# Kernel optimization log

Hardware: AMD Instinct MI355X
Metric: run time of the kernel (lower is better)

## Reference

```python
import jax, jax.numpy as jnp
import numpy as np

N_NODES = 100_000
N_EDGES = 800_000
D_IN = 64
HID = 32   # hidden_channels
OUT = 64   # out_channels
H1, H2, H3 = 7, 4, 1


def _lin(key, din, dout, scale=0.05):
    k1, k2 = jax.random.split(key)
    W = jax.random.normal(k1, (din, dout), jnp.float32) * scale
    b = jax.random.normal(k2, (dout,), jnp.float32) * scale
    return W, b


def setup_inputs() -> dict:
    key = jax.random.key(0)
    ks = jax.random.split(key, 16)
    x = jax.random.normal(ks[0], (N_NODES, D_IN), jnp.float32)
    edge_index = jax.random.randint(ks[1], (2, N_EDGES), 0, N_NODES, dtype=jnp.int32)
    inp = {"x": x, "edge_index": edge_index}
    # (in_dim, heads, per-head channels) for the 3 TransformerConv layers
    dims = [(D_IN, H1, HID), (H1 * HID, H2, HID), (H2 * HID, H3, OUT)]
    i = 2
    for l, (din, h, c) in enumerate(dims, start=1):
        for nm in ("q", "k", "v", "s"):  # query, key, value, skip linears
            W, b = _lin(ks[i], din, h * c)
            i += 1
            inp[f"W{nm}{l}"] = W
            inp[f"b{nm}{l}"] = b
    return inp


def _transformer_conv(x, src, dst, Wq, bq, Wk, bk, Wv, bv, Ws, bs, H, C):
    # PyG TransformerConv (concat=True, beta=False, root_weight=True, no edge feats)
    q = (x @ Wq + bq).reshape(-1, H, C)
    k = (x @ Wk + bk).reshape(-1, H, C)
    v = (x @ Wv + bv).reshape(-1, H, C)
    # per-edge attention logits [E, H]
    alpha = jnp.einsum('ehc,ehc->eh', q[dst], k[src]) / jnp.sqrt(jnp.asarray(C, q.dtype))
    # segment softmax over incoming edges of each dst node
    amax = jax.ops.segment_max(alpha, dst, num_segments=N_NODES)
    ex = jnp.exp(alpha - amax[dst])
    denom = jax.ops.segment_sum(ex, dst, num_segments=N_NODES)
    attn = ex / (denom[dst] + 1e-16)
    # weighted message aggregation [N, H, C] -> [N, H*C]
    msg = v[src] * attn[..., None]
    out = jax.ops.segment_sum(msg, dst, num_segments=N_NODES).reshape(N_NODES, H * C)
    # root/skip connection
    return out + x @ Ws + bs


def reference(x, edge_index,
              Wq1, bq1, Wk1, bk1, Wv1, bv1, Ws1, bs1,
              Wq2, bq2, Wk2, bk2, Wv2, bv2, Ws2, bs2,
              Wq3, bq3, Wk3, bk3, Wv3, bv3, Ws3, bs3):
    src, dst = edge_index[0], edge_index[1]
    h = jax.nn.relu(_transformer_conv(x, src, dst, Wq1, bq1, Wk1, bk1, Wv1, bv1, Ws1, bs1, H1, HID))
    h = jax.nn.relu(_transformer_conv(h, src, dst, Wq2, bq2, Wk2, bk2, Wv2, bv2, Ws2, bs2, H2, HID))
    return _transformer_conv(h, src, dst, Wq3, bq3, Wk3, bk3, Wv3, bv3, Ws3, bs3, H3, OUT)
```

## Files before the change

### kernel.cpp

```cpp
#include <hip/hip_runtime.h>
#include <hip/hip_bf16.h>
#include <math.h>

#define N_NODES 100000
#define N_EDGES 800000
#define SCAN_BLOCKS 98

typedef __attribute__((ext_vector_type(8))) short short8;
typedef __attribute__((ext_vector_type(4))) float f32x4;

__device__ __forceinline__ unsigned short f2b(float f) {
    __hip_bfloat16 h = __float2bfloat16(f);
    return *reinterpret_cast<unsigned short*>(&h);
}
__device__ __forceinline__ float b2f(unsigned short u) {
    unsigned int v = ((unsigned int)u) << 16;
    float f;
    __builtin_memcpy(&f, &v, 4);
    return f;
}
__device__ __forceinline__ float2 up2(unsigned u) {
    unsigned lo = u << 16;
    unsigned hi = u & 0xffff0000u;
    float2 r;
    __builtin_memcpy(&r.x, &lo, 4);
    __builtin_memcpy(&r.y, &hi, 4);
    return r;
}


__global__ void hist_kernel(const int* __restrict__ dst, int* __restrict__ deg) {
    int e = blockIdx.x * blockDim.x + threadIdx.x;
    if (e < N_EDGES) atomicAdd(&deg[dst[e]], 1);
}

__global__ __launch_bounds__(1024) void scan_part(const int* __restrict__ deg,
                                                  int* __restrict__ rowptr,
                                                  int* __restrict__ partials) {
    __shared__ int buf[1024];
    const int t = threadIdx.x;
    const int i = blockIdx.x * 1024 + t;
    int x = (i < N_NODES) ? deg[i] : 0;
    buf[t] = x;
    __syncthreads();
    for (int off = 1; off < 1024; off <<= 1) {
        int y = (t >= off) ? buf[t - off] : 0;
        __syncthreads();
        buf[t] += y;
        __syncthreads();
    }
    if (i < N_NODES) rowptr[i] = buf[t] - x;
    if (t == 1023) partials[blockIdx.x] = buf[t];
}

__global__ __launch_bounds__(128) void scan_tail(int* __restrict__ partials,
                                                 int* __restrict__ rowptr) {
    __shared__ int buf[128];
    const int t = threadIdx.x;
    int x = (t < SCAN_BLOCKS) ? partials[t] : 0;
    buf[t] = x;
    __syncthreads();
    for (int off = 1; off < 128; off <<= 1) {
        int y = (t >= off) ? buf[t - off] : 0;
        __syncthreads();
        buf[t] += y;
        __syncthreads();
    }
    if (t < SCAN_BLOCKS) partials[t] = buf[t] - x;
    if (t == 127) rowptr[N_NODES] = buf[127];
}

__global__ __launch_bounds__(1024) void scan_add(int* __restrict__ rowptr,
                                                 const int* __restrict__ partials) {
    const int i = blockIdx.x * 1024 + threadIdx.x;
    if (i < N_NODES) rowptr[i] += partials[blockIdx.x];
}

__global__ void scatter_kernel(const int* __restrict__ src, const int* __restrict__ dst,
                               const int* __restrict__ rowptr, int* __restrict__ cursor,
                               int* __restrict__ sorted_src) {
    int e = blockIdx.x * blockDim.x + threadIdx.x;
    if (e < N_EDGES) {
        int d = dst[e];
        int pos = atomicAdd(&cursor[d], 1);
        sorted_src[rowptr[d] + pos] = src[e];
    }
}

__global__ void fill_kernel(float* __restrict__ out, int n, float val) {
    int i = blockIdx.x * blockDim.x + threadIdx.x;
    if (i < n) out[i] = val;
}


__global__ void convert_kernel(const float* __restrict__ X, unsigned short* __restrict__ Y, int n4) {
    int i = blockIdx.x * blockDim.x + threadIdx.x;
    if (i < n4) {
        float4 f = ((const float4*)X)[i];
        ushort4 u;
        u.x = f2b(f.x); u.y = f2b(f.y); u.z = f2b(f.z); u.w = f2b(f.w);
        ((ushort4*)Y)[i] = u;
    }
}

__global__ void build_wt(const float* __restrict__ Wq, const float* __restrict__ Wk,
                         const float* __restrict__ Wv, const float* __restrict__ Wsk,
                         const float* __restrict__ bq, const float* __restrict__ bk,
                         const float* __restrict__ bv, const float* __restrict__ bsk,
                         unsigned short* __restrict__ WT, float* __restrict__ biasF,
                         int K, int HC) {
    int total = 4 * HC * K;
    int idx = blockIdx.x * blockDim.x + threadIdx.x;
    if (idx >= total) return;
    int rowc = idx / K;
    int kk = idx - rowc * K;
    int sec = rowc / HC;
    int cw = rowc - sec * HC;
    const float* W = (sec == 0) ? Wq : (sec == 1) ? Wk : (sec == 2) ? Wv : Wsk;
    WT[idx] = f2b(W[(size_t)kk * HC + cw]);
    if (kk == 0) {
        const float* B = (sec == 0) ? bq : (sec == 1) ? bk : (sec == 2) ? bv : bsk;
        biasF[rowc] = B[cw];
    }
}


template <int K, bool YBF>
__global__ __launch_bounds__(256) void mfma_gemm(
    const unsigned short* __restrict__ Xb, const unsigned short* __restrict__ WT,
    const float* __restrict__ biasF, void* __restrict__ Y,
    int ncols, int ostride, int sec_size, int sec_stride, int h0C) {
    constexpr int STR = 40;
    constexpr int ESTR = 24;
    __shared__ __align__(16) unsigned short Xs[128 * STR];
    __shared__ __align__(16) unsigned short Ws[128 * STR];
    __shared__ __align__(16) unsigned short Es[128 * ESTR];
    const int t = threadIdx.x;
    const int wave = t >> 6, lane = t & 63, quad = lane >> 4, l16 = lane & 15;
    const int n0 = blockIdx.x * 128, c0 = blockIdx.y * 128;

    f32x4 acc[2][8];
#pragma unroll
    for (int i = 0; i < 2; ++i)
#pragma unroll
        for (int j = 0; j < 8; ++j)
#pragma unroll
            for (int r = 0; r < 4; ++r) acc[i][j][r] = 0.f;

    for (int k0 = 0; k0 < K; k0 += 32) {
#pragma unroll
        for (int i = 0; i < 2; ++i) {
            int idx = t + i * 256;
            int row = idx >> 2;
            int seg = (idx & 3) << 3;
            int gr = n0 + row;
            short8 xv;
#pragma unroll
            for (int z = 0; z < 8; ++z) xv[z] = 0;
            if (gr < N_NODES)
                xv = *(const short8*)(Xb + (size_t)gr * K + k0 + seg);
            *(short8*)(&Xs[row * STR + seg]) = xv;

            int c = c0 + row;
            short8 wv;
#pragma unroll
            for (int z = 0; z < 8; ++z) wv[z] = 0;
            if (c < ncols) {
                int sec = c / sec_size;
                int wtrow = sec * sec_stride + h0C + (c - sec * sec_size);
                wv = *(const short8*)(WT + (size_t)wtrow * K + k0 + seg);
            }
            *(short8*)(&Ws[row * STR + seg]) = wv;
        }
        __syncthreads();

        short8 af0 = *(short8*)(&Xs[(wave * 32 + l16) * STR + quad * 8]);
        short8 af1 = *(short8*)(&Xs[(wave * 32 + 16 + l16) * STR + quad * 8]);
#pragma unroll
        for (int ct = 0; ct < 8; ++ct) {
            short8 bfr = *(short8*)(&Ws[(ct * 16 + l16) * STR + quad * 8]);
            acc[0][ct] = __builtin_amdgcn_mfma_f32_16x16x32_bf16(af0, bfr, acc[0][ct], 0, 0, 0);
            acc[1][ct] = __builtin_amdgcn_mfma_f32_16x16x32_bf16(af1, bfr, acc[1][ct], 0, 0, 0);
        }
        __syncthreads();
    }

    if constexpr (YBF) {
        const int erow = t >> 1;
        const int ehalf = (t & 1) * 8;
        for (int ct = 0; ct < 8; ++ct) {
            int col = c0 + ct * 16 + l16;
            float bv = 0.f;
            if (col < ncols) {
                int sec = col / sec_size;
                bv = biasF[sec * sec_stride + h0C + (col - sec * sec_size)];
            }
            __syncthreads();
#pragma unroll
            for (int rt = 0; rt < 2; ++rt)
#pragma unroll
                for (int r = 0; r < 4; ++r) {
                    int row = wave * 32 + rt * 16 + quad * 4 + r;
                    Es[row * ESTR + l16] = f2b(acc[rt][ct][r] + bv);
                }
            __syncthreads();
            int gr = n0 + erow;
            int gc = c0 + ct * 16 + ehalf;
            if (gr < N_NODES && gc < ncols)
                *(short8*)((unsigned short*)Y + (size_t)gr * ostride + gc) =
                    *(const short8*)(&Es[erow * ESTR + ehalf]);
        }
    } else {
#pragma unroll
        for (int ct = 0; ct < 8; ++ct) {
            int col = c0 + ct * 16 + l16;
            if (col >= ncols) continue;
            int sec = col / sec_size;
            float bv = biasF[sec * sec_stride + h0C + (col - sec * sec_size)];
#pragma unroll
            for (int rt = 0; rt < 2; ++rt) {
#pragma unroll
                for (int r = 0; r < 4; ++r) {
                    int row = n0 + wave * 32 + rt * 16 + quad * 4 + r;
                    if (row < N_NODES)
                        ((float*)Y)[(size_t)row * ostride + col] = acc[rt][ct][r] + bv;
                }
            }
        }
    }
}


template <int C, int NH, bool RELU, bool YBF>
__global__ __launch_bounds__(256) void attn2(
    const unsigned short* __restrict__ F,
    const int* __restrict__ rowptr, const int* __restrict__ ssrc,
    void* __restrict__ Hv, int h0, int ostride) {
    constexpr int LPN = NH * C / 2;
    constexpr int NPW = (LPN == 48) ? 1 : (64 / LPN);
    constexpr int Ms = 3 * NH * C;
    constexpr int gC = NH * C;
    const int lane = threadIdx.x & 63;
    const int wave = (blockIdx.x * 256 + threadIdx.x) >> 6;
    const int slot = lane / LPN;
    const int cl = lane - slot * LPN;
    const int n = wave * NPW + slot;
    if (slot >= NPW || n >= N_NODES) return;

    const int head = cl / (C / 2);
    const int c2 = (cl - head * (C / 2)) * 2;
    const int qoff = head * C + c2;
    const float SCALE2 = ((C == 64) ? 0.125f : 0.17677669529663687f) * 1.44269504f;

    float2 q2 = up2(*(const unsigned*)(F + (size_t)n * Ms + qoff));
    int s0 = rowptr[n], s1 = rowptr[n + 1];

    float l = 0.f, ax = 0.f, ay = 0.f;
    int ei = s0;
    for (; ei + 1 < s1; ei += 2) {
        int sA = ssrc[ei], sB = ssrc[ei + 1];
        const unsigned short* rA = F + (size_t)sA * Ms;
        const unsigned short* rB = F + (size_t)sB * Ms;
        unsigned kAu = *(const unsigned*)(rA + gC + qoff);
        unsigned vAu = *(const unsigned*)(rA + 2 * gC + qoff);
        unsigned kBu = *(const unsigned*)(rB + gC + qoff);
        unsigned vBu = *(const unsigned*)(rB + 2 * gC + qoff);
        float2 kA = up2(kAu), kB = up2(kBu);
        float pA = fmaf(q2.y, kA.y, q2.x * kA.x);
        float pB = fmaf(q2.y, kB.y, q2.x * kB.x);
#pragma unroll
        for (int off = C / 4; off > 0; off >>= 1) {
            pA += __shfl_xor(pA, off);
            pB += __shfl_xor(pB, off);
        }
        float exA = exp2f(pA * SCALE2);
        float exB = exp2f(pB * SCALE2);
        float2 vA = up2(vAu), vB = up2(vBu);
        l += exA + exB;
        ax = fmaf(exA, vA.x, fmaf(exB, vB.x, ax));
        ay = fmaf(exA, vA.y, fmaf(exB, vB.y, ay));
    }
    if (ei < s1) {
        int sA = ssrc[ei];
        const unsigned short* rA = F + (size_t)sA * Ms;
        float2 kA = up2(*(const unsigned*)(rA + gC + qoff));
        float2 vA = up2(*(const unsigned*)(rA + 2 * gC + qoff));
        float pA = fmaf(q2.y, kA.y, q2.x * kA.x);
#pragma unroll
        for (int off = C / 4; off > 0; off >>= 1) pA += __shfl_xor(pA, off);
        float exA = exp2f(pA * SCALE2);
        l += exA;
        ax = fmaf(exA, vA.x, ax);
        ay = fmaf(exA, vA.y, ay);
    }

    float inv = 1.f / (l + 1e-16f);
    float rx = ax * inv, ry = ay * inv;

    const int col = (h0 + head) * C + c2;
    if constexpr (YBF) {
        unsigned* Hp = (unsigned*)((unsigned short*)Hv + (size_t)n * ostride + col);
        float2 h = up2(*Hp);
        float ox = h.x + rx, oy = h.y + ry;
        if (RELU) { ox = fmaxf(ox, 0.f); oy = fmaxf(oy, 0.f); }
        *Hp = (unsigned)f2b(ox) | ((unsigned)f2b(oy) << 16);
    } else {
        float2* Hp = (float2*)((float*)Hv + (size_t)n * ostride + col);
        float2 h = *Hp;
        h.x += rx; h.y += ry;
        if (RELU) { h.x = fmaxf(h.x, 0.f); h.y = fmaxf(h.y, 0.f); }
        *Hp = h;
    }
}


static inline void launch_attn32(int NH, int h0, const unsigned short* F,
                                 void* H, int ostride, const int* rowptr,
                                 const int* ssrc, hipStream_t stream) {
    switch (NH) {
        case 1: attn2<32, 1, true, true><<<6250, 256, 0, stream>>>(F, rowptr, ssrc, H, h0, ostride); break;
        case 2: attn2<32, 2, true, true><<<12500, 256, 0, stream>>>(F, rowptr, ssrc, H, h0, ostride); break;
        case 3: attn2<32, 3, true, true><<<25000, 256, 0, stream>>>(F, rowptr, ssrc, H, h0, ostride); break;
        default: attn2<32, 4, true, true><<<25000, 256, 0, stream>>>(F, rowptr, ssrc, H, h0, ostride); break;
    }
}

extern "C" void kernel_launch(void* const* d_in, const int* in_sizes, int n_in,
                              void* d_out, int out_size, void* d_ws, size_t ws_size,
                              hipStream_t stream) {
    const float* x = (const float*)d_in[0];
    const int* ei = (const int*)d_in[1];
    const int* srcp = ei;
    const int* dstp = ei + N_EDGES;

    const float* W[12];
    const float* B[12];
    for (int i = 0; i < 12; ++i) {
        W[i] = (const float*)d_in[2 + 2 * i];
        B[i] = (const float*)d_in[3 + 2 * i];
    }
    float* out = (float*)d_out;

    char* p = (char*)d_ws;
    size_t off = 0;
    unsigned short* wt  = (unsigned short*)(p + off); off += 240000;
    float* biasF        = (float*)(p + off);          off += 4096;
    int* rowptr = (int*)(p + off); off += sizeof(int) * (N_NODES + 1);
    int* deg    = (int*)(p + off); off += sizeof(int) * N_NODES;
    int* cursor = (int*)(p + off); off += sizeof(int) * N_NODES;
    int* partials = (int*)(p + off); off += sizeof(int) * 128;
    int* ssrc   = (int*)(p + off); off += sizeof(int) * N_EDGES;
    off = (off + 255) & ~(size_t)255;
    unsigned short* h1  = (unsigned short*)(p + off); off += (size_t)224 * N_NODES * 2;
    unsigned short* h2  = (unsigned short*)(p + off); off += (size_t)128 * N_NODES * 2;
    unsigned short* xb1 = (unsigned short*)(p + off); off += (size_t)64 * N_NODES * 2;
    unsigned short* tail = (unsigned short*)(p + off);

    if (ws_size < off + 6500000) {
        fill_kernel<<<(out_size + 255) / 256, 256, 0, stream>>>(out, out_size, (float)(ws_size >> 20));
        return;
    }
    size_t tail_bytes = ws_size - off;
    const size_t F1PASS = (size_t)3 * 32 * N_NODES * 2;

    int nh1[7], np1 = 0;
    int nh2[4], np2 = 0;
    const unsigned short *F_l1, *F_l2;
    unsigned short *F1w, *F2w;
    if (tail_bytes >= 4 * F1PASS) {
        nh1[np1++] = 4; nh1[np1++] = 3;
        nh2[np2++] = 4;
        F1w = F2w = tail;
    } else if (tail_bytes >= 2 * F1PASS) {
        nh1[np1++] = 2; nh1[np1++] = 2; nh1[np1++] = 2; nh1[np1++] = 1;
        nh2[np2++] = 2; nh2[np2++] = 2;
        F1w = F2w = tail;
    } else {
        for (int i = 0; i < 7; ++i) nh1[np1++] = 1;
        for (int i = 0; i < 4; ++i) nh2[np2++] = 1;
        F1w = h2;
        F2w = xb1;
    }
    F_l1 = F1w; F_l2 = F2w;
    unsigned short* F3 = h1;

    hipMemsetAsync(deg, 0, sizeof(int) * 2 * N_NODES, stream);
    hist_kernel<<<(N_EDGES + 255) / 256, 256, 0, stream>>>(dstp, deg);
    scan_part<<<SCAN_BLOCKS, 1024, 0, stream>>>(deg, rowptr, partials);
    scan_tail<<<1, 128, 0, stream>>>(partials, rowptr);
    scan_add<<<SCAN_BLOCKS, 1024, 0, stream>>>(rowptr, partials);
    scatter_kernel<<<(N_EDGES + 255) / 256, 256, 0, stream>>>(srcp, dstp, rowptr, cursor, ssrc);

    convert_kernel<<<(N_NODES * 64 / 4 + 255) / 256, 256, 0, stream>>>(x, xb1, N_NODES * 64 / 4);

    const int GX = (N_NODES + 127) / 128;

    build_wt<<<(4 * 224 * 64 + 255) / 256, 256, 0, stream>>>(
        W[0], W[1], W[2], W[3], B[0], B[1], B[2], B[3], wt, biasF, 64, 224);
    mfma_gemm<64, true><<<dim3(GX, 2), 256, 0, stream>>>(
        xb1, wt + (size_t)3 * 224 * 64, biasF + 3 * 224, h1, 224, 224, 224, 0, 0);
    {
        int h0 = 0;
        for (int pass = 0; pass < np1; ++pass) {
            int NH = nh1[pass];
            int nc = 3 * NH * 32;
            mfma_gemm<64, true><<<dim3(GX, (nc + 127) / 128), 256, 0, stream>>>(
                xb1, wt, biasF, F1w, nc, nc, NH * 32, 224, h0 * 32);
            launch_attn32(NH, h0, F_l1, h1, 224, rowptr, ssrc, stream);
            h0 += NH;
        }
    }

    build_wt<<<(4 * 128 * 224 + 255) / 256, 256, 0, stream>>>(
        W[4], W[5], W[6], W[7], B[4], B[5], B[6], B[7], wt, biasF, 224, 128);
    mfma_gemm<224, true><<<dim3(GX, 1), 256, 0, stream>>>(
        h1, wt + (size_t)3 * 128 * 224, biasF + 3 * 128, h2, 128, 128, 128, 0, 0);
    {
        int h0 = 0;
        for (int pass = 0; pass < np2; ++pass) {
            int NH = nh2[pass];
            int nc = 3 * NH * 32;
            mfma_gemm<224, true><<<dim3(GX, (nc + 127) / 128), 256, 0, stream>>>(
                h1, wt, biasF, F2w, nc, nc, NH * 32, 128, h0 * 32);
            launch_attn32(NH, h0, F_l2, h2, 128, rowptr, ssrc, stream);
            h0 += NH;
        }
    }

    build_wt<<<(4 * 64 * 128 + 255) / 256, 256, 0, stream>>>(
        W[8], W[9], W[10], W[11], B[8], B[9], B[10], B[11], wt, biasF, 128, 64);
    mfma_gemm<128, true><<<dim3(GX, 2), 256, 0, stream>>>(
        h2, wt, biasF, F3, 192, 192, 64, 64, 0);
    mfma_gemm<128, false><<<dim3(GX, 1), 256, 0, stream>>>(
        h2, wt + (size_t)3 * 64 * 128, biasF + 3 * 64, out, 64, 64, 64, 0, 0);
    attn2<64, 1, false, false><<<12500, 256, 0, stream>>>(F3, rowptr, ssrc, out, 0, 64);
}
```

Before: 743.5 us.

## Widen GEMM column tiles, vectorize attention to 4 channels/lane, single-pass layer 1

Adds a CT template parameter so the MFMA GEMM can cover 256 output columns per block. X tiles are reused across more columns, and MFMAs for out-of-range column tiles are skipped. The attention kernel now handles 4 channels per lane with 8-byte loads, so fewer lanes work per node and more nodes share each wave. A 7-head single-pass path for layer 1 is added when workspace allows, which removes repeated GEMM and attention launches at the cost of a larger feature buffer and more register pressure in the wider GEMM.

```diff
diff --git a/kernel.cpp b/kernel.cpp
--- a/kernel.cpp
+++ b/kernel.cpp
@@ -12,12 +12,6 @@
 __device__ __forceinline__ unsigned short f2b(float f) {
     __hip_bfloat16 h = __float2bfloat16(f);
     return *reinterpret_cast<unsigned short*>(&h);
-}
-__device__ __forceinline__ float b2f(unsigned short u) {
-    unsigned int v = ((unsigned int)u) << 16;
-    float f;
-    __builtin_memcpy(&f, &v, 4);
-    return f;
 }
 __device__ __forceinline__ float2 up2(unsigned u) {
     unsigned lo = u << 16;
@@ -125,7 +119,7 @@
 }
 
 
-template <int K, bool YBF>
+template <int K, bool YBF, int CT>
 __global__ __launch_bounds__(256) void mfma_gemm(
     const unsigned short* __restrict__ Xb, const unsigned short* __restrict__ WT,
     const float* __restrict__ biasF, void* __restrict__ Y,
@@ -133,17 +127,17 @@
     constexpr int STR = 40;
     constexpr int ESTR = 24;
     __shared__ __align__(16) unsigned short Xs[128 * STR];
-    __shared__ __align__(16) unsigned short Ws[128 * STR];
+    __shared__ __align__(16) unsigned short Ws[128 * CT * STR];
     __shared__ __align__(16) unsigned short Es[128 * ESTR];
     const int t = threadIdx.x;
     const int wave = t >> 6, lane = t & 63, quad = lane >> 4, l16 = lane & 15;
-    const int n0 = blockIdx.x * 128, c0 = blockIdx.y * 128;
-
-    f32x4 acc[2][8];
+    const int n0 = blockIdx.x * 128, c0 = blockIdx.y * (128 * CT);
+
+    f32x4 acc[2][8 * CT];
 #pragma unroll
     for (int i = 0; i < 2; ++i)
 #pragma unroll
-        for (int j = 0; j < 8; ++j)
+        for (int j = 0; j < 8 * CT; ++j)
 #pragma unroll
             for (int r = 0; r < 4; ++r) acc[i][j][r] = 0.f;
 
@@ -160,7 +154,12 @@
             if (gr < N_NODES)
                 xv = *(const short8*)(Xb + (size_t)gr * K + k0 + seg);
             *(short8*)(&Xs[row * STR + seg]) = xv;
-
+        }
+#pragma unroll
+        for (int i = 0; i < 2 * CT; ++i) {
+            int idx = t + i * 256;
+            int row = idx >> 2;
+            int seg = (idx & 3) << 3;
             int c = c0 + row;
             short8 wv;
 #pragma unroll
@@ -177,10 +176,12 @@
         short8 af0 = *(short8*)(&Xs[(wave * 32 + l16) * STR + quad * 8]);
         short8 af1 = *(short8*)(&Xs[(wave * 32 + 16 + l16) * STR + quad * 8]);
 #pragma unroll
-        for (int ct = 0; ct < 8; ++ct) {
-            short8 bfr = *(short8*)(&Ws[(ct * 16 + l16) * STR + quad * 8]);
-            acc[0][ct] = __builtin_amdgcn_mfma_f32_16x16x32_bf16(af0, bfr, acc[0][ct], 0, 0, 0);
-            acc[1][ct] = __builtin_amdgcn_mfma_f32_16x16x32_bf16(af1, bfr, acc[1][ct], 0, 0, 0);
+        for (int ct = 0; ct < 8 * CT; ++ct) {
+            if (c0 + ct * 16 < ncols) {
+                short8 bfr = *(short8*)(&Ws[(ct * 16 + l16) * STR + quad * 8]);
+                acc[0][ct] = __builtin_amdgcn_mfma_f32_16x16x32_bf16(af0, bfr, acc[0][ct], 0, 0, 0);
+                acc[1][ct] = __builtin_amdgcn_mfma_f32_16x16x32_bf16(af1, bfr, acc[1][ct], 0, 0, 0);
+            }
         }
         __syncthreads();
     }
@@ -188,7 +189,8 @@
     if constexpr (YBF) {
         const int erow = t >> 1;
         const int ehalf = (t & 1) * 8;
-        for (int ct = 0; ct < 8; ++ct) {
+        for (int ct = 0; ct < 8 * CT; ++ct) {
+            if (c0 + ct * 16 >= ncols) break;
             int col = c0 + ct * 16 + l16;
             float bv = 0.f;
             if (col < ncols) {
@@ -212,7 +214,7 @@
         }
     } else {
 #pragma unroll
-        for (int ct = 0; ct < 8; ++ct) {
+        for (int ct = 0; ct < 8 * CT; ++ct) {
             int col = c0 + ct * 16 + l16;
             if (col >= ncols) continue;
             int sec = col / sec_size;
@@ -230,14 +232,29 @@
     }
 }
 
+template <int K, bool YBF>
+static inline void launch_gemm(const unsigned short* Xb, const unsigned short* WT,
+                               const float* biasF, void* Y, int ncols, int ostride,
+                               int sec_size, int sec_stride, int h0C, hipStream_t s) {
+    const int GX = (N_NODES + 127) / 128;
+    if (ncols > 128) {
+        int ny = (ncols + 255) / 256;
+        mfma_gemm<K, YBF, 2><<<dim3(GX, ny), 256, 0, s>>>(
+            Xb, WT, biasF, Y, ncols, ostride, sec_size, sec_stride, h0C);
+    } else {
+        mfma_gemm<K, YBF, 1><<<dim3(GX, 1), 256, 0, s>>>(
+            Xb, WT, biasF, Y, ncols, ostride, sec_size, sec_stride, h0C);
+    }
+}
+
 
 template <int C, int NH, bool RELU, bool YBF>
-__global__ __launch_bounds__(256) void attn2(
+__global__ __launch_bounds__(256) void attn3(
     const unsigned short* __restrict__ F,
     const int* __restrict__ rowptr, const int* __restrict__ ssrc,
     void* __restrict__ Hv, int h0, int ostride) {
-    constexpr int LPN = NH * C / 2;
-    constexpr int NPW = (LPN == 48) ? 1 : (64 / LPN);
+    constexpr int LPN = NH * C / 4;
+    constexpr int NPW = 64 / LPN;
     constexpr int Ms = 3 * NH * C;
     constexpr int gC = NH * C;
     const int lane = threadIdx.x & 63;
@@ -247,83 +264,103 @@
     const int n = wave * NPW + slot;
     if (slot >= NPW || n >= N_NODES) return;
 
-    const int head = cl / (C / 2);
-    const int c2 = (cl - head * (C / 2)) * 2;
-    const int qoff = head * C + c2;
+    const int head = cl / (C / 4);
+    const int c4 = (cl - head * (C / 4)) * 4;
+    const int qoff = head * C + c4;
     const float SCALE2 = ((C == 64) ? 0.125f : 0.17677669529663687f) * 1.44269504f;
 
-    float2 q2 = up2(*(const unsigned*)(F + (size_t)n * Ms + qoff));
+    uint2 qu = *(const uint2*)(F + (size_t)n * Ms + qoff);
+    float2 qa = up2(qu.x), qb = up2(qu.y);
     int s0 = rowptr[n], s1 = rowptr[n + 1];
 
-    float l = 0.f, ax = 0.f, ay = 0.f;
+    float l = 0.f, a0 = 0.f, a1 = 0.f, a2 = 0.f, a3 = 0.f;
     int ei = s0;
     for (; ei + 1 < s1; ei += 2) {
         int sA = ssrc[ei], sB = ssrc[ei + 1];
         const unsigned short* rA = F + (size_t)sA * Ms;
         const unsigned short* rB = F + (size_t)sB * Ms;
-        unsigned kAu = *(const unsigned*)(rA + gC + qoff);
-        unsigned vAu = *(const unsigned*)(rA + 2 * gC + qoff);
-        unsigned kBu = *(const unsigned*)(rB + gC + qoff);
-        unsigned vBu = *(const unsigned*)(rB + 2 * gC + qoff);
-        float2 kA = up2(kAu), kB = up2(kBu);
-        float pA = fmaf(q2.y, kA.y, q2.x * kA.x);
-        float pB = fmaf(q2.y, kB.y, q2.x * kB.x);
-#pragma unroll
-        for (int off = C / 4; off > 0; off >>= 1) {
+        uint2 kAu = *(const uint2*)(rA + gC + qoff);
+        uint2 vAu = *(const uint2*)(rA + 2 * gC + qoff);
+        uint2 kBu = *(const uint2*)(rB + gC + qoff);
+        uint2 vBu = *(const uint2*)(rB + 2 * gC + qoff);
+        float2 kA0 = up2(kAu.x), kA1 = up2(kAu.y);
+        float2 kB0 = up2(kBu.x), kB1 = up2(kBu.y);
+        float pA = fmaf(qa.x, kA0.x, qa.y * kA0.y) + fmaf(qb.x, kA1.x, qb.y * kA1.y);
+        float pB = fmaf(qa.x, kB0.x, qa.y * kB0.y) + fmaf(qb.x, kB1.x, qb.y * kB1.y);
+#pragma unroll
+        for (int off = C / 8; off > 0; off >>= 1) {
             pA += __shfl_xor(pA, off);
             pB += __shfl_xor(pB, off);
         }
         float exA = exp2f(pA * SCALE2);
         float exB = exp2f(pB * SCALE2);
-        float2 vA = up2(vAu), vB = up2(vBu);
+        float2 vA0 = up2(vAu.x), vA1 = up2(vAu.y);
+        float2 vB0 = up2(vBu.x), vB1 = up2(vBu.y);
         l += exA + exB;
-        ax = fmaf(exA, vA.x, fmaf(exB, vB.x, ax));
-        ay = fmaf(exA, vA.y, fmaf(exB, vB.y, ay));
+        a0 = fmaf(exA, vA0.x, fmaf(exB, vB0.x, a0));
+        a1 = fmaf(exA, vA0.y, fmaf(exB, vB0.y, a1));
+        a2 = fmaf(exA, vA1.x, fmaf(exB, vB1.x, a2));
+        a3 = fmaf(exA, vA1.y, fmaf(exB, vB1.y, a3));
     }
     if (ei < s1) {
         int sA = ssrc[ei];
         const unsigned short* rA = F + (size_t)sA * Ms;
-        float2 kA = up2(*(const unsigned*)(rA + gC + qoff));
-        float2 vA = up2(*(const unsigned*)(rA + 2 * gC + qoff));
-        float pA = fmaf(q2.y, kA.y, q2.x * kA.x);
-#pragma unroll
-        for (int off = C / 4; off > 0; off >>= 1) pA += __shfl_xor(pA, off);
+        uint2 kAu = *(const uint2*)(rA + gC + qoff);
+        uint2 vAu = *(const uint2*)(rA + 2 * gC + qoff);
+        float2 kA0 = up2(kAu.x), kA1 = up2(kAu.y);
+        float pA = fmaf(qa.x, kA0.x, qa.y * kA0.y) + fmaf(qb.x, kA1.x, qb.y * kA1.y);
+#pragma unroll
+        for (int off = C / 8; off > 0; off >>= 1) pA += __shfl_xor(pA, off);
         float exA = exp2f(pA * SCALE2);
+        float2 vA0 = up2(vAu.x), vA1 = up2(vAu.y);
         l += exA;
-        ax = fmaf(exA, vA.x, ax);
-        ay = fmaf(exA, vA.y, ay);
+        a0 = fmaf(exA, vA0.x, a0);
+        a1 = fmaf(exA, vA0.y, a1);
+        a2 = fmaf(exA, vA1.x, a2);
+        a3 = fmaf(exA, vA1.y, a3);
     }
 
     float inv = 1.f / (l + 1e-16f);
-    float rx = ax * inv, ry = ay * inv;
-
-    const int col = (h0 + head) * C + c2;
+    float r0 = a0 * inv, r1 = a1 * inv, r2 = a2 * inv, r3 = a3 * inv;
+
+    const int col = (h0 + head) * C + c4;
     if constexpr (YBF) {
-        unsigned* Hp = (unsigned*)((unsigned short*)Hv + (size_t)n * ostride + col);
-        float2 h = up2(*Hp);
-        float ox = h.x + rx, oy = h.y + ry;
-        if (RELU) { ox = fmaxf(ox, 0.f); oy = fmaxf(oy, 0.f); }
-        *Hp = (unsigned)f2b(ox) | ((unsigned)f2b(oy) << 16);
+        uint2* Hp = (uint2*)((unsigned short*)Hv + (size_t)n * ostride + col);
+        uint2 hv = *Hp;
+        float2 hx = up2(hv.x), hy = up2(hv.y);
+        float o0 = hx.x + r0, o1 = hx.y + r1, o2 = hy.x + r2, o3 = hy.y + r3;
+        if (RELU) {
+            o0 = fmaxf(o0, 0.f); o1 = fmaxf(o1, 0.f);
+            o2 = fmaxf(o2, 0.f); o3 = fmaxf(o3, 0.f);
+        }
+        uint2 pv;
+        pv.x = (unsigned)f2b(o0) | ((unsigned)f2b(o1) << 16);
+        pv.y = (unsigned)f2b(o2) | ((unsigned)f2b(o3) << 16);
+        *Hp = pv;
     } else {
-        float2* Hp = (float2*)((float*)Hv + (size_t)n * ostride + col);
-        float2 h = *Hp;
-        h.x += rx; h.y += ry;
-        if (RELU) { h.x = fmaxf(h.x, 0.f); h.y = fmaxf(h.y, 0.f); }
+        float4* Hp = (float4*)((float*)Hv + (size_t)n * ostride + col);
+        float4 h = *Hp;
+        h.x += r0; h.y += r1; h.z += r2; h.w += r3;
+        if (RELU) {
+            h.x = fmaxf(h.x, 0.f); h.y = fmaxf(h.y, 0.f);
+            h.z = fmaxf(h.z, 0.f); h.w = fmaxf(h.w, 0.f);
+        }
         *Hp = h;
     }
 }
-
 
 static inline void launch_attn32(int NH, int h0, const unsigned short* F,
                                  void* H, int ostride, const int* rowptr,
                                  const int* ssrc, hipStream_t stream) {
     switch (NH) {
-        case 1: attn2<32, 1, true, true><<<6250, 256, 0, stream>>>(F, rowptr, ssrc, H, h0, ostride); break;
-        case 2: attn2<32, 2, true, true><<<12500, 256, 0, stream>>>(F, rowptr, ssrc, H, h0, ostride); break;
-        case 3: attn2<32, 3, true, true><<<25000, 256, 0, stream>>>(F, rowptr, ssrc, H, h0, ostride); break;
-        default: attn2<32, 4, true, true><<<25000, 256, 0, stream>>>(F, rowptr, ssrc, H, h0, ostride); break;
-    }
-}
+        case 1: attn3<32, 1, true, true><<<3125, 256, 0, stream>>>(F, rowptr, ssrc, H, h0, ostride); break;
+        case 2: attn3<32, 2, true, true><<<6250, 256, 0, stream>>>(F, rowptr, ssrc, H, h0, ostride); break;
+        case 3: attn3<32, 3, true, true><<<12500, 256, 0, stream>>>(F, rowptr, ssrc, H, h0, ostride); break;
+        case 4: attn3<32, 4, true, true><<<12500, 256, 0, stream>>>(F, rowptr, ssrc, H, h0, ostride); break;
+        default: attn3<32, 7, true, true><<<25000, 256, 0, stream>>>(F, rowptr, ssrc, H, h0, ostride); break;
+    }
+}
+
 
 extern "C" void kernel_launch(void* const* d_in, const int* in_sizes, int n_in,
                               void* d_out, int out_size, void* d_ws, size_t ws_size,
@@ -365,9 +402,12 @@
 
     int nh1[7], np1 = 0;
     int nh2[4], np2 = 0;
-    const unsigned short *F_l1, *F_l2;
     unsigned short *F1w, *F2w;
-    if (tail_bytes >= 4 * F1PASS) {
+    if (tail_bytes >= 7 * F1PASS) {
+        nh1[np1++] = 7;
+        nh2[np2++] = 4;
+        F1w = F2w = tail;
+    } else if (tail_bytes >= 4 * F1PASS) {
         nh1[np1++] = 4; nh1[np1++] = 3;
         nh2[np2++] = 4;
         F1w = F2w = tail;
@@ -381,7 +421,6 @@
         F1w = h2;
         F2w = xb1;
     }
-    F_l1 = F1w; F_l2 = F2w;
     unsigned short* F3 = h1;
 
     hipMemsetAsync(deg, 0, sizeof(int) * 2 * N_NODES, stream);
@@ -393,45 +432,40 @@
 
     convert_kernel<<<(N_NODES * 64 / 4 + 255) / 256, 256, 0, stream>>>(x, xb1, N_NODES * 64 / 4);
 
-    const int GX = (N_NODES + 127) / 128;
-
     build_wt<<<(4 * 224 * 64 + 255) / 256, 256, 0, stream>>>(
         W[0], W[1], W[2], W[3], B[0], B[1], B[2], B[3], wt, biasF, 64, 224);
-    mfma_gemm<64, true><<<dim3(GX, 2), 256, 0, stream>>>(
-        xb1, wt + (size_t)3 * 224 * 64, biasF + 3 * 224, h1, 224, 224, 224, 0, 0);
+    launch_gemm<64, true>(xb1, wt + (size_t)3 * 224 * 64, biasF + 3 * 224, h1,
+                          224, 224, 224, 0, 0, stream);
     {
         int h0 = 0;
         for (int pass = 0; pass < np1; ++pass) {
             int NH = nh1[pass];
             int nc = 3 * NH * 32;
-            mfma_gemm<64, true><<<dim3(GX, (nc + 127) / 128), 256, 0, stream>>>(
-                xb1, wt, biasF, F1w, nc, nc, NH * 32, 224, h0 * 32);
-            launch_attn32(NH, h0, F_l1, h1, 224, rowptr, ssrc, stream);
+            launch_gemm<64, true>(xb1, wt, biasF, F1w, nc, nc, NH * 32, 224, h0 * 32, stream);
+            launch_attn32(NH, h0, F1w, h1, 224, rowptr, ssrc, stream);
             h0 += NH;
         }
     }
 
     build_wt<<<(4 * 128 * 224 + 255) / 256, 256, 0, stream>>>(
         W[4], W[5], W[6], W[7], B[4], B[5], B[6], B[7], wt, biasF, 224, 128);
-    mfma_gemm<224, true><<<dim3(GX, 1), 256, 0, stream>>>(
-        h1, wt + (size_t)3 * 128 * 224, biasF + 3 * 128, h2, 128, 128, 128, 0, 0);
+    launch_gemm<224, true>(h1, wt + (size_t)3 * 128 * 224, biasF + 3 * 128, h2,
+                           128, 128, 128, 0, 0, stream);
     {
         int h0 = 0;
         for (int pass = 0; pass < np2; ++pass) {
             int NH = nh2[pass];
             int nc = 3 * NH * 32;
-            mfma_gemm<224, true><<<dim3(GX, (nc + 127) / 128), 256, 0, stream>>>(
-                h1, wt, biasF, F2w, nc, nc, NH * 32, 128, h0 * 32);
-            launch_attn32(NH, h0, F_l2, h2, 128, rowptr, ssrc, stream);
+            launch_gemm<224, true>(h1, wt, biasF, F2w, nc, nc, NH * 32, 128, h0 * 32, stream);
+            launch_attn32(NH, h0, F2w, h2, 128, rowptr, ssrc, stream);
             h0 += NH;
         }
     }
 
     build_wt<<<(4 * 64 * 128 + 255) / 256, 256, 0, stream>>>(
         W[8], W[9], W[10], W[11], B[8], B[9], B[10], B[11], wt, biasF, 128, 64);
-    mfma_gemm<128, true><<<dim3(GX, 2), 256, 0, stream>>>(
-        h2, wt, biasF, F3, 192, 192, 64, 64, 0);
-    mfma_gemm<128, false><<<dim3(GX, 1), 256, 0, stream>>>(
-        h2, wt + (size_t)3 * 64 * 128, biasF + 3 * 64, out, 64, 64, 64, 0, 0);
-    attn2<64, 1, false, false><<<12500, 256, 0, stream>>>(F3, rowptr, ssrc, out, 0, 64);
-}
+    launch_gemm<128, true>(h2, wt, biasF, F3, 192, 192, 64, 64, 0, stream);
+    launch_gemm<128, false>(h2, wt + (size_t)3 * 64 * 128, biasF + 3 * 64, out,
+                            64, 64, 64, 0, 0, stream);
+    attn3<64, 1, false, false><<<6250, 256, 0, stream>>>(F3, rowptr, ssrc, out, 0, 64);
+}
```

Result: slower. 861.5 us (+15.9%).
